# Performance work log

Hardware: AMD Instinct MI355X
Metric: run time of the kernel (lower is better)

## Reference

```python
import jax, jax.numpy as jnp
import numpy as np

B, L, D, H, R, E = 4, 2048, 256, 4, 128, 32768
HD = D // H  # head dim of long-range attention
FF = 4 * D   # positionwise FFN hidden
NEG_SLOPE = 0.2  # GATConv leaky_relu slope


def setup_inputs() -> dict:
    key = jax.random.key(0)
    ks = jax.random.split(key, 16)
    n = lambda k, sh: jax.random.normal(k, sh, dtype=jnp.float32) * 0.05
    z = lambda sh: jnp.zeros(sh, dtype=jnp.float32)
    o = lambda sh: jnp.ones(sh, dtype=jnp.float32)
    return {
        "s": jax.random.normal(ks[0], (B, L, D), dtype=jnp.float32),
        "gat_W": n(ks[1], (D, H * D)),
        "gat_att_src": n(ks[2], (H, D)),
        "gat_att_dst": n(ks[3], (H, D)),
        "gat_b": z((H * D,)),
        "short_W": n(ks[4], (H * D, D)), "short_b": z((D,)),
        "q_W": n(ks[5], (D, D)), "q_b": z((D,)),
        "k_W": n(ks[6], (D, D)), "k_b": z((D,)),
        "v_W": n(ks[7], (D, D)), "v_b": z((D,)),
        "o_W": n(ks[8], (D, D)), "o_b": z((D,)),
        "p_W": n(ks[9], (D, R)), "p_b": z((R,)),
        "lnq_g": o((D,)), "lnq_b": z((D,)),
        "lnk_g": o((D,)), "lnk_b": z((D,)),
        "lnv_g": o((D,)), "lnv_b": z((D,)),
        "ln1_g": o((D,)), "ln1_b": z((D,)),
        "ln2_g": o((D,)), "ln2_b": z((D,)),
        "f1_W": n(ks[10], (D, FF)), "f1_b": z((FF,)),
        "f2_W": n(ks[11], (FF, D)), "f2_b": z((D,)),
        "edge_index": jax.random.randint(ks[12], (2, E), 0, L, dtype=jnp.int32),
    }


def _ln(x, g, b, eps=1e-5):
    mu = jnp.mean(x, -1, keepdims=True)
    var = jnp.mean(jnp.square(x - mu), -1, keepdims=True)
    return (x - mu) * jax.lax.rsqrt(var + eps) * g + b


def _forward(p, edge_index):
    s = p["s"]
    loop = jnp.arange(L, dtype=edge_index.dtype)  # add_self_loops=True
    src = jnp.concatenate([edge_index[0], loop])
    dst = jnp.concatenate([edge_index[1], loop])

    def gat_one(x):  # x: [L, D] -> [L, H*D]  (PyG GATConv, concat=True)
        h = (x @ p["gat_W"]).reshape(L, H, D)
        a_src = jnp.einsum("nhc,hc->nh", h, p["gat_att_src"])
        a_dst = jnp.einsum("nhc,hc->nh", h, p["gat_att_dst"])
        e = jax.nn.leaky_relu(a_src[src] + a_dst[dst], NEG_SLOPE)  # [Etot, H]
        m = jax.ops.segment_max(e, dst, num_segments=L)            # scatter softmax
        ex = jnp.exp(e - m[dst])
        den = jax.ops.segment_sum(ex, dst, num_segments=L)
        alpha = ex / den[dst]
        out = jax.ops.segment_sum(h[src] * alpha[:, :, None], dst, num_segments=L)
        return out.reshape(L, H * D) + p["gat_b"]

    short = jax.vmap(gat_one)(s) @ p["short_W"] + p["short_b"]  # [B,L,D]

    # DynamicLongRange (Linformer-style dynamic projection)
    q = _ln(s @ p["q_W"] + p["q_b"], p["lnq_g"], p["lnq_b"])
    k = _ln(s @ p["k_W"] + p["k_b"], p["lnk_g"], p["lnk_b"])
    v = _ln(s @ p["v_W"] + p["v_b"], p["lnv_g"], p["lnv_b"])
    pm = jax.nn.softmax(k @ p["p_W"] + p["p_b"], axis=1)          # [B,L,R], softmax over seq
    k_c = jnp.einsum("blr,bld->brd", pm, k).reshape(B, R, H, HD)
    v_c = jnp.einsum("blr,bld->brd", pm, v).reshape(B, R, H, HD)
    q_h = q.reshape(B, L, H, HD)
    scores = jnp.einsum("blhd,brhd->bhlr", q_h, k_c) / jnp.sqrt(jnp.float32(HD))
    probs = jax.nn.softmax(scores, axis=-1)
    lng = jnp.einsum("bhlr,brhd->blhd", probs, v_c).reshape(B, L, D)
    lng = lng @ p["o_W"] + p["o_b"]

    # fuse short + long, residual + LN, then positionwise FFN + residual + LN
    h1 = _ln(s + short + lng, p["ln1_g"], p["ln1_b"])
    ff = jax.nn.relu(h1 @ p["f1_W"] + p["f1_b"]) @ p["f2_W"] + p["f2_b"]
    return _ln(h1 + ff, p["ln2_g"], p["ln2_b"])


def reference(s, gat_W, gat_att_src, gat_att_dst, gat_b, short_W, short_b,
              q_W, q_b, k_W, k_b, v_W, v_b, o_W, o_b, p_W, p_b,
              lnq_g, lnq_b, lnk_g, lnk_b, lnv_g, lnv_b,
              ln1_g, ln1_b, ln2_g, ln2_b, f1_W, f1_b, f2_W, f2_b, edge_index):
    p = dict(s=s, gat_W=gat_W, gat_att_src=gat_att_src, gat_att_dst=gat_att_dst,
             gat_b=gat_b, short_W=short_W, short_b=short_b, q_W=q_W, q_b=q_b,
             k_W=k_W, k_b=k_b, v_W=v_W, v_b=v_b, o_W=o_W, o_b=o_b, p_W=p_W,
             p_b=p_b, lnq_g=lnq_g, lnq_b=lnq_b, lnk_g=lnk_g, lnk_b=lnk_b,
             lnv_g=lnv_g, lnv_b=lnv_b, ln1_g=ln1_g, ln1_b=ln1_b, ln2_g=ln2_g,
             ln2_b=ln2_b, f1_W=f1_W, f1_b=f1_b, f2_W=f2_W, f2_b=f2_b)
    return _forward(p, edge_index)
```

## Files before the change

### kernel.cpp

```cpp
#include <hip/hip_runtime.h>
#include <math.h>

#define BB   4
#define LSEQ 2048
#define DV   256
#define HH   4
#define RR   128
#define EE   32768
#define ETOT (EE + LSEQ)
#define FFD  1024

typedef unsigned short u16;
typedef __attribute__((ext_vector_type(8))) short bf16x8;
typedef __attribute__((ext_vector_type(4))) float f32x4;

__device__ __forceinline__ u16 f2bf(float f) {
    union { float f; unsigned u; } x; x.f = f;
    unsigned r = x.u + 0x7fff + ((x.u >> 16) & 1);
    return (u16)(r >> 16);
}
__device__ __forceinline__ float bf2f(u16 u) {
    union { unsigned u; float f; } x; x.u = ((unsigned)u) << 16;
    return x.f;
}

__device__ __forceinline__ void gload16(const void* g, void* l) {
    __builtin_amdgcn_global_load_lds(
        (const __attribute__((address_space(1))) unsigned int*)g,
        (__attribute__((address_space(3))) unsigned int*)l, 16, 0, 0);
}

template<int BM, int BN, int OUTBF16, int ACT>
__global__ __launch_bounds__(256) void mfma_gemm_k(
    const u16* __restrict__ A, const u16* __restrict__ BT,
    const float* __restrict__ bias, void* __restrict__ Cv,
    int M, int N, int K, int lda, int ldb, int ldc,
    long bsA1, long bsA2, long bsB1, long bsB2, long bsC1, long bsC2,
    int subH, long pairB, long pairC, int ksl, int split, float alpha)
{
    constexpr int BK = 64;
    __shared__ u16 As[BM * BK];
    __shared__ u16 Bs[BN * BK];

    int z = blockIdx.z;
    int zb = z / subH, zh = z - zb * subH;
    int mtiles = M / BM;
    int pair = blockIdx.y / mtiles;
    int mt   = blockIdx.y - pair * mtiles;

    const u16* Ab = A  + zb * bsA1 + zh * bsA2;
    const u16* Bb = BT + zb * bsB1 + zh * bsB2 + (long)pair * pairB;
    int kstart = split ? zh * ksl : 0;
    int kcount = split ? ksl : K;
    int m0 = mt * BM, n0 = blockIdx.x * BN;

    int tid  = threadIdx.x;
    int wave = tid >> 6, lane = tid & 63;
    constexpr int WGN = (BN == 128) ? 2 : 1;
    constexpr int WGM = 4 / WGN;
    constexpr int MI  = BM / (WGM * 16);
    constexpr int NI  = BN / (WGN * 16);
    int wm = wave / WGN, wn = wave - wm * WGN;
    int wmo = wm * (MI * 16);
    int wno = wn * (NI * 16);

    f32x4 acc[MI][NI];
#pragma unroll
    for (int mi = 0; mi < MI; ++mi)
#pragma unroll
        for (int ni = 0; ni < NI; ++ni)
            acc[mi][ni] = (f32x4){0.f, 0.f, 0.f, 0.f};

    constexpr int AIT = (BM * BK / 8) / 256;
    constexpr int BIT = (BN * BK / 8) / 256;

    for (int k0 = 0; k0 < kcount; k0 += BK) {
        int kb = kstart + k0;
#pragma unroll
        for (int i = 0; i < AIT; ++i) {
            int p   = i * 256 + tid;
            int row = p >> 3;
            int kc  = (p & 7) ^ (row & 7);
            const u16* gp = Ab + (long)(m0 + row) * lda + kb + kc * 8;
            gload16(gp, (char*)As + (size_t)(i * 256 + wave * 64) * 16);
        }
#pragma unroll
        for (int i = 0; i < BIT; ++i) {
            int p   = i * 256 + tid;
            int row = p >> 3;
            int kc  = (p & 7) ^ (row & 7);
            const u16* gp = Bb + (long)(n0 + row) * ldb + kb + kc * 8;
            gload16(gp, (char*)Bs + (size_t)(i * 256 + wave * 64) * 16);
        }
        asm volatile("s_waitcnt vmcnt(0)");
        __syncthreads();

        const char* Ac = (const char*)As;
        const char* Bc = (const char*)Bs;
#pragma unroll
        for (int kh = 0; kh < 2; ++kh) {
            bf16x8 af[MI], bfr[NI];
            int kby = kh * 64 + ((lane >> 4) << 4);
#pragma unroll
            for (int mi = 0; mi < MI; ++mi) {
                int r = wmo + mi * 16 + (lane & 15);
                af[mi] = *(const bf16x8*)(Ac + r * 128 + (kby ^ ((r & 7) << 4)));
            }
#pragma unroll
            for (int ni = 0; ni < NI; ++ni) {
                int r = wno + ni * 16 + (lane & 15);
                bfr[ni] = *(const bf16x8*)(Bc + r * 128 + (kby ^ ((r & 7) << 4)));
            }
#pragma unroll
            for (int mi = 0; mi < MI; ++mi)
#pragma unroll
                for (int ni = 0; ni < NI; ++ni)
                    acc[mi][ni] = __builtin_amdgcn_mfma_f32_16x16x32_bf16(
                        af[mi], bfr[ni], acc[mi][ni], 0, 0, 0);
        }
        __syncthreads();
    }

    long cb = zb * bsC1 + zh * bsC2 + (long)pair * pairC;
#pragma unroll
    for (int mi = 0; mi < MI; ++mi) {
#pragma unroll
        for (int ni = 0; ni < NI; ++ni) {
            int col = n0 + wno + ni * 16 + (lane & 15);
            float bv = bias ? bias[col] : 0.f;
#pragma unroll
            for (int j = 0; j < 4; ++j) {
                int row = m0 + wmo + mi * 16 + ((lane >> 4) << 2) + j;
                float v = acc[mi][ni][j] * alpha + bv;
                if (ACT) v = fmaxf(v, 0.f);
                long idx = (long)row * ldc + col + cb;
                if (OUTBF16) ((u16*)Cv)[idx] = f2bf(v);
                else         ((float*)Cv)[idx] = v;
            }
        }
    }
}

template<int MODE>
__global__ __launch_bounds__(256) void gemm_ln_k(
    const u16* __restrict__ A, const u16* __restrict__ BT,
    const float* __restrict__ bias, int K, int lda,
    const float* __restrict__ lg0, const float* __restrict__ lb0,
    const float* __restrict__ lg1, const float* __restrict__ lb1,
    const float* __restrict__ lg2, const float* __restrict__ lb2,
    const float* __restrict__ resF, const u16* __restrict__ resB,
    u16* __restrict__ outRM, u16* __restrict__ outRM2,
    u16* __restrict__ outT, float* __restrict__ outF)
{
    constexpr int BK = 64;
    __shared__ char smem[40960];
    __shared__ float redS[64][4], redQ[64][4];
    u16* Asm = (u16*)smem;
    u16* Bsm = (u16*)(smem + 8192);

    int seg = blockIdx.x;
    int m0 = blockIdx.y * 64;
    int n0 = seg * 256;
    int tid = threadIdx.x, wave = tid >> 6, lane = tid & 63;
    int c = lane & 15, g = lane >> 4;

    f32x4 acc[4][4];
#pragma unroll
    for (int mi = 0; mi < 4; ++mi)
#pragma unroll
        for (int ni = 0; ni < 4; ++ni)
            acc[mi][ni] = (f32x4){0.f, 0.f, 0.f, 0.f};

    for (int k0 = 0; k0 < K; k0 += BK) {
#pragma unroll
        for (int i = 0; i < 2; ++i) {
            int p   = i * 256 + tid;
            int row = p >> 3;
            int kc  = (p & 7) ^ (row & 7);
            gload16(A + (long)(m0 + row) * lda + k0 + kc * 8,
                    smem + (size_t)(i * 256 + wave * 64) * 16);
        }
#pragma unroll
        for (int i = 0; i < 8; ++i) {
            int p   = i * 256 + tid;
            int row = p >> 3;
            int kc  = (p & 7) ^ (row & 7);
            gload16(BT + (long)(n0 + row) * K + k0 + kc * 8,
                    smem + 8192 + (size_t)(i * 256 + wave * 64) * 16);
        }
        asm volatile("s_waitcnt vmcnt(0)");
        __syncthreads();

        const char* Ac = (const char*)Asm;
        const char* Bc = (const char*)Bsm;
#pragma unroll
        for (int kh = 0; kh < 2; ++kh) {
            bf16x8 af[4], bfr[4];
            int kby = kh * 64 + (g << 4);
#pragma unroll
            for (int mi = 0; mi < 4; ++mi) {
                int r = mi * 16 + c;
                af[mi] = *(const bf16x8*)(Ac + r * 128 + (kby ^ ((r & 7) << 4)));
            }
#pragma unroll
            for (int ni = 0; ni < 4; ++ni) {
                int r = wave * 64 + ni * 16 + c;
                bfr[ni] = *(const bf16x8*)(Bc + r * 128 + (kby ^ ((r & 7) << 4)));
            }
#pragma unroll
            for (int mi = 0; mi < 4; ++mi)
#pragma unroll
                for (int ni = 0; ni < 4; ++ni)
                    acc[mi][ni] = __builtin_amdgcn_mfma_f32_16x16x32_bf16(
                        af[mi], bfr[ni], acc[mi][ni], 0, 0, 0);
        }
        __syncthreads();
    }

#pragma unroll
    for (int mi = 0; mi < 4; ++mi)
#pragma unroll
        for (int ni = 0; ni < 4; ++ni) {
            int colL = wave * 64 + ni * 16 + c;
            float bv = bias[n0 + colL];
#pragma unroll
            for (int j = 0; j < 4; ++j) {
                int row = mi * 16 + g * 4 + j;
                float v = acc[mi][ni][j] + bv;
                if (MODE == 1) {
                    long idx = (long)(m0 + row) * 256 + colL;
                    v += resF[idx] + bf2f(resB[idx]);
                }
                if (MODE == 2) {
                    long idx = (long)(m0 + row) * 256 + colL;
                    v += bf2f(resB[idx]);
                }
                acc[mi][ni][j] = v;
            }
        }

#pragma unroll
    for (int mi = 0; mi < 4; ++mi)
#pragma unroll
        for (int j = 0; j < 4; ++j) {
            float s1 = 0.f, q1 = 0.f;
#pragma unroll
            for (int ni = 0; ni < 4; ++ni) {
                float v = acc[mi][ni][j];
                s1 += v; q1 += v * v;
            }
#pragma unroll
            for (int m = 1; m <= 8; m <<= 1) {
                s1 += __shfl_xor(s1, m);
                q1 += __shfl_xor(q1, m);
            }
            if (c == 0) {
                int row = mi * 16 + g * 4 + j;
                redS[row][wave] = s1;
                redQ[row][wave] = q1;
            }
        }
    __syncthreads();

    const float* gam;
    const float* bet;
    if (MODE == 0) {
        gam = (seg == 0) ? lg0 : (seg == 1) ? lg1 : lg2;
        bet = (seg == 0) ? lb0 : (seg == 1) ? lb1 : lb2;
    } else { gam = lg0; bet = lb0; }

    u16* T = (u16*)smem;

    float gv[4], bv2[4];
#pragma unroll
    for (int ni = 0; ni < 4; ++ni) {
        int colL = wave * 64 + ni * 16 + c;
        gv[ni] = gam[colL];
        bv2[ni] = bet[colL];
    }

#pragma unroll
    for (int mi = 0; mi < 4; ++mi)
#pragma unroll
        for (int j = 0; j < 4; ++j) {
            int row = mi * 16 + g * 4 + j;
            float S = redS[row][0] + redS[row][1] + redS[row][2] + redS[row][3];
            float Q = redQ[row][0] + redQ[row][1] + redQ[row][2] + redQ[row][3];
            float mu = S * (1.0f / 256.f);
            float var = Q * (1.0f / 256.f) - mu * mu;
            float rs = rsqrtf(var + 1e-5f);
#pragma unroll
            for (int ni = 0; ni < 4; ++ni) {
                int colL = wave * 64 + ni * 16 + c;
                float o = (acc[mi][ni][j] - mu) * rs * gv[ni] + bv2[ni];
                long idx = (long)(m0 + row) * 256 + colL;
                if (MODE == 0) {
                    u16 ob = f2bf(o);
                    if (seg == 0)      outRM[idx]  = ob;
                    else if (seg == 1) { outRM2[idx] = ob; T[colL * 65 + row] = ob; }
                    else               T[colL * 65 + row] = ob;
                } else if (MODE == 1) {
                    outRM[idx] = f2bf(o);
                } else {
                    outF[idx] = o;
                }
            }
        }

    if (MODE == 0 && seg >= 1) {
        __syncthreads();
        int b = m0 >> 11;
        int l0 = m0 & 2047;
        u16* dst = outT + ((seg == 2) ? 2097152 : 0)
                 + (long)b * 524288 + (long)tid * 2048 + l0;
        const u16* src = T + tid * 65;
#pragma unroll
        for (int i = 0; i < 8; ++i) {
            u16 tmp[8];
#pragma unroll
            for (int k2 = 0; k2 < 8; ++k2) tmp[k2] = src[i * 8 + k2];
            *(uint4*)(dst + i * 8) = *(uint4*)tmp;
        }
    }
}

__global__ __launch_bounds__(256) void attn_k(
    const u16* __restrict__ qb, const u16* __restrict__ kcb,
    const u16* __restrict__ vcT, u16* __restrict__ lngb)
{
    __shared__ u16 Ps[64 * 128];

    int bh = blockIdx.y;
    int b = bh >> 2, h = bh & 3;
    int l0 = blockIdx.x * 64;
    int tid = threadIdx.x, wave = tid >> 6, lane = tid & 63;
    int c = lane & 15, g = lane >> 4;

    const u16* kc = kcb + (long)b * (RR * DV) + h * 64;
    const u16* qg = qb + ((long)(b * LSEQ + l0)) * DV + h * 64;
    const u16* vg = vcT + ((long)b * DV + h * 64) * RR;

    f32x4 acc[8];
#pragma unroll
    for (int mi = 0; mi < 8; ++mi) acc[mi] = (f32x4){0.f, 0.f, 0.f, 0.f};

#pragma unroll
    for (int kh = 0; kh < 2; ++kh) {
        bf16x8 bq = *(const bf16x8*)(qg + (long)(wave * 16 + c) * DV + kh * 32 + g * 8);
#pragma unroll
        for (int mi = 0; mi < 8; ++mi) {
            bf16x8 af = *(const bf16x8*)(kc + (long)(mi * 16 + c) * DV + kh * 32 + g * 8);
            acc[mi] = __builtin_amdgcn_mfma_f32_16x16x32_bf16(af, bq, acc[mi], 0, 0, 0);
        }
    }

    float mx = -INFINITY;
#pragma unroll
    for (int mi = 0; mi < 8; ++mi)
#pragma unroll
        for (int j = 0; j < 4; ++j) {
            acc[mi][j] *= 0.125f;
            mx = fmaxf(mx, acc[mi][j]);
        }
    mx = fmaxf(mx, __shfl_xor(mx, 16));
    mx = fmaxf(mx, __shfl_xor(mx, 32));
    float den = 0.f;
#pragma unroll
    for (int mi = 0; mi < 8; ++mi)
#pragma unroll
        for (int j = 0; j < 4; ++j) {
            acc[mi][j] = __expf(acc[mi][j] - mx);
            den += acc[mi][j];
        }
    den += __shfl_xor(den, 16);
    den += __shfl_xor(den, 32);
    float inv = 1.0f / den;

    int l = wave * 16 + c;
#pragma unroll
    for (int mi = 0; mi < 8; ++mi) {
        short4 sv;
        sv.x = (short)f2bf(acc[mi][0] * inv);
        sv.y = (short)f2bf(acc[mi][1] * inv);
        sv.z = (short)f2bf(acc[mi][2] * inv);
        sv.w = (short)f2bf(acc[mi][3] * inv);
        int byte = l * 256 + ((mi * 32 + g * 8) ^ ((l & 7) << 4));
        *(short4*)((char*)Ps + byte) = sv;
    }
    __syncthreads();

    f32x4 a2[4];
#pragma unroll
    for (int ni = 0; ni < 4; ++ni) a2[ni] = (f32x4){0.f, 0.f, 0.f, 0.f};
#pragma unroll
    for (int kb = 0; kb < 4; ++kb) {
        int kby = kb * 64 + (g << 4);
        bf16x8 pa = *(const bf16x8*)((char*)Ps + l * 256 + (kby ^ ((l & 7) << 4)));
#pragma unroll
        for (int ni = 0; ni < 4; ++ni) {
            bf16x8 vf = *(const bf16x8*)(vg + (long)(ni * 16 + c) * RR + kb * 32 + g * 8);
            a2[ni] = __builtin_amdgcn_mfma_f32_16x16x32_bf16(pa, vf, a2[ni], 0, 0, 0);
        }
    }
#pragma unroll
    for (int ni = 0; ni < 4; ++ni)
#pragma unroll
        for (int j = 0; j < 4; ++j) {
            int lr = wave * 16 + g * 4 + j;
            int dh = ni * 16 + c;
            lngb[((long)(b * LSEQ + l0 + lr)) * DV + h * 64 + dh] = f2bf(a2[ni][j]);
        }
}

struct WTD { const float* src; u16* dst; int K, N, toff; };
struct WTA { WTD d[9]; };

__global__ __launch_bounds__(256) void wtrans_all_k(WTA a)
{
    int bid = blockIdx.x;
    int di = 0;
#pragma unroll
    for (int i = 1; i < 9; ++i) if (bid >= a.d[i].toff) di = i;
    const float* src = a.d[di].src;
    u16* dst = a.d[di].dst;
    int K = a.d[di].K, N = a.d[di].N;
    int tix = bid - a.d[di].toff;
    int nx = N >> 5;
    int tn = tix % nx, tk = tix / nx;
    int n0 = tn * 32, k0 = tk * 32;

    __shared__ float t[32][33];
    int tx = threadIdx.x & 31, ty = threadIdx.x >> 5;
#pragma unroll
    for (int i = 0; i < 32; i += 8)
        t[ty + i][tx] = src[(long)(k0 + ty + i) * N + n0 + tx];
    __syncthreads();
#pragma unroll
    for (int i = 0; i < 32; i += 8)
        dst[(long)(n0 + ty + i) * K + k0 + tx] = f2bf(t[tx][ty + i]);
}

__global__ void castcat_k(const float* __restrict__ in, u16* __restrict__ out,
                          const float* qb_, const float* kb_, const float* vb_,
                          float* qkvb, int* icnt)
{
    int bid = blockIdx.x;
    if (bid < 2048) {
        int i = (bid * 256 + threadIdx.x) * 4;
        float4 v = *(const float4*)(in + i);
        out[i]     = f2bf(v.x);
        out[i + 1] = f2bf(v.y);
        out[i + 2] = f2bf(v.z);
        out[i + 3] = f2bf(v.w);
    } else if (bid == 2048) {
        int i = threadIdx.x;
#pragma unroll
        for (int rep = 0; rep < 3; ++rep) {
            int j = i + rep * 256;
            qkvb[j] = (j < 256) ? qb_[j] : ((j < 512) ? kb_[j - 256] : vb_[j - 512]);
        }
    } else {
        int t = (bid - 2049) * 256 + threadIdx.x;
        if (t < 512) ((int4*)icnt)[t] = (int4){0, 0, 0, 0};
    }
}

__global__ __launch_bounds__(256) void gat_att_k(
    const u16* __restrict__ h, const float* __restrict__ att_src,
    const float* __restrict__ att_dst, float* __restrict__ a_src,
    float* __restrict__ a_dst)
{
    int row  = blockIdx.x * 4 + (threadIdx.x >> 6);
    int lane = threadIdx.x & 63;
    int c0   = lane * 16;
    int head = lane >> 4;

    float as[16], ad[16];
#pragma unroll
    for (int i = 0; i < 16; ++i) { as[i] = att_src[c0 + i]; ad[i] = att_dst[c0 + i]; }

    const u16* hr = h + (long)row * (HH * DV) + c0;
    bf16x8 v0 = *(const bf16x8*)(hr);
    bf16x8 v1 = *(const bf16x8*)(hr + 8);
    float ps = 0.f, pd = 0.f;
#pragma unroll
    for (int i = 0; i < 8; ++i) {
        float f0 = bf2f((u16)v0[i]), f1 = bf2f((u16)v1[i]);
        ps += f0 * as[i] + f1 * as[i + 8];
        pd += f0 * ad[i] + f1 * ad[i + 8];
    }
#pragma unroll
    for (int m = 1; m <= 8; m <<= 1) {
        ps += __shfl_xor(ps, m);
        pd += __shfl_xor(pd, m);
    }
    if ((lane & 15) == 0) {
        a_src[(long)row * HH + head] = ps;
        a_dst[(long)row * HH + head] = pd;
    }
}

__global__ void csr_count_k(const int* __restrict__ ei, int* __restrict__ cnt)
{
    int i = blockIdx.x * blockDim.x + threadIdx.x;
    if (i >= ETOT) return;
    int dst = (i < EE) ? ei[EE + i] : (i - EE);
    atomicAdd(&cnt[dst], 1);
}

__global__ __launch_bounds__(256) void csr_scan_k(const int* __restrict__ cnt, int* __restrict__ off)
{
    __shared__ int chunk[256];
    int tid = threadIdx.x;
    int base = tid * 8;
    int loc[8];
    int s = 0;
#pragma unroll
    for (int i = 0; i < 8; ++i) { loc[i] = s; s += cnt[base + i]; }
    chunk[tid] = s;
    __syncthreads();
    for (int st = 1; st < 256; st <<= 1) {
        int v = (tid >= st) ? chunk[tid - st] : 0;
        __syncthreads();
        chunk[tid] += v;
        __syncthreads();
    }
    int pre = (tid == 0) ? 0 : chunk[tid - 1];
#pragma unroll
    for (int i = 0; i < 8; ++i) off[base + i] = pre + loc[i];
    if (tid == 255) off[LSEQ] = chunk[255];
}

__global__ void csr_fill_k(const int* __restrict__ ei, const int* __restrict__ off,
                           int* __restrict__ cnt, int* __restrict__ bucket)
{
    int i = blockIdx.x * blockDim.x + threadIdx.x;
    if (i >= ETOT) return;
    int dst = (i < EE) ? ei[EE + i] : (i - EE);
    int p = atomicSub(&cnt[dst], 1) - 1;
    bucket[off[dst] + p] = i;
}

__global__ __launch_bounds__(256) void gat_gather_k(
    const u16* __restrict__ h, const int* __restrict__ ei,
    const int* __restrict__ off, const int* __restrict__ bucket,
    const float* __restrict__ a_src, const float* __restrict__ a_dst,
    const float* __restrict__ gat_b, u16* __restrict__ out)
{
    int wv = threadIdx.x >> 6, lane = threadIdx.x & 63;
    int n = blockIdx.x * 4 + wv;
    int b = blockIdx.y;
    int beg = off[n], deg = off[n + 1] - beg;

    __shared__ int   src_sh[4][64];
    __shared__ float ex_sh[4][64][4];

    const float* asrc_b = a_src + (long)b * LSEQ * HH;
    const float4 ad4 = *(const float4*)(a_dst + ((long)b * LSEQ + n) * HH);
    float adst[4] = { ad4.x, ad4.y, ad4.z, ad4.w };

    int hd = lane >> 4;
    const u16* hb = h + (long)b * LSEQ * (HH * DV) + lane * 16;
    float acc[16];
#pragma unroll
    for (int i = 0; i < 16; ++i) acc[i] = 0.f;
    float sm[4] = { 0.f, 0.f, 0.f, 0.f };

    for (int c0 = 0; c0 < deg; c0 += 64) {
        int idx = c0 + lane;
        if (idx < deg) {
            int eid = bucket[beg + idx];
            int src = (eid < EE) ? ei[eid] : (eid - EE);
            src_sh[wv][lane] = src;
            float4 as4 = *(const float4*)(asrc_b + (long)src * HH);
            float as[4] = { as4.x, as4.y, as4.z, as4.w };
#pragma unroll
            for (int hh = 0; hh < 4; ++hh) {
                float e = as[hh] + adst[hh];
                e = (e >= 0.f) ? e : 0.2f * e;
                float ex = __expf(e);
                ex_sh[wv][lane][hh] = ex;
                sm[hh] += ex;
            }
        }
        int cn = deg - c0; if (cn > 64) cn = 64;
#pragma unroll 2
        for (int j = 0; j < cn; ++j) {
            int src = src_sh[wv][j];
            float al = ex_sh[wv][j][hd];
            const u16* p = hb + (long)src * (HH * DV);
            bf16x8 v0 = *(const bf16x8*)p;
            bf16x8 v1 = *(const bf16x8*)(p + 8);
#pragma unroll
            for (int i = 0; i < 8; ++i) {
                acc[i]     += al * bf2f((u16)v0[i]);
                acc[i + 8] += al * bf2f((u16)v1[i]);
            }
        }
    }

#pragma unroll
    for (int hh = 0; hh < 4; ++hh)
#pragma unroll
        for (int m = 32; m >= 1; m >>= 1)
            sm[hh] += __shfl_xor(sm[hh], m);
    float inv = 1.0f / sm[hd];

    u16 o16[16];
    const float* gb = gat_b + lane * 16;
#pragma unroll
    for (int i = 0; i < 16; ++i) o16[i] = f2bf(acc[i] * inv + gb[i]);
    uint4* op = (uint4*)(out + ((long)b * LSEQ + n) * (HH * DV) + lane * 16);
    op[0] = ((uint4*)o16)[0];
    op[1] = ((uint4*)o16)[1];
}

__global__ __launch_bounds__(256) void colsoftmax_k(const float* __restrict__ pm,
                                                    u16* __restrict__ pmT)
{
    int r = blockIdx.x;
    int b = blockIdx.y;
    int tid = threadIdx.x, wave = tid >> 6, lane = tid & 63;
    const float* base = pm + (long)b * LSEQ * RR + r;
    u16* obase = pmT + ((long)b * RR + r) * LSEQ;

    float x[8];
#pragma unroll
    for (int i = 0; i < 8; ++i) x[i] = base[(long)(tid + i * 256) * RR];

    __shared__ float red[4];
    __shared__ float m_sh, d_sh;
    float mx = x[0];
#pragma unroll
    for (int i = 1; i < 8; ++i) mx = fmaxf(mx, x[i]);
#pragma unroll
    for (int m = 32; m >= 1; m >>= 1) mx = fmaxf(mx, __shfl_xor(mx, m));
    if (lane == 0) red[wave] = mx;
    __syncthreads();
    if (tid == 0) m_sh = fmaxf(fmaxf(red[0], red[1]), fmaxf(red[2], red[3]));
    __syncthreads();
    float m = m_sh;
    float sm = 0.f;
#pragma unroll
    for (int i = 0; i < 8; ++i) { x[i] = __expf(x[i] - m); sm += x[i]; }
#pragma unroll
    for (int mm = 32; mm >= 1; mm >>= 1) sm += __shfl_xor(sm, mm);
    if (lane == 0) red[wave] = sm;
    __syncthreads();
    if (tid == 0) d_sh = red[0] + red[1] + red[2] + red[3];
    __syncthreads();
    float inv = 1.0f / d_sh;
#pragma unroll
    for (int i = 0; i < 8; ++i) obase[tid + i * 256] = f2bf(x[i] * inv);
}

__global__ __launch_bounds__(256) void reduce_kvc_k(
    const float* __restrict__ part, u16* __restrict__ kvcb, u16* __restrict__ vcT)
{
    int pb = blockIdx.z;
    int pair = pb >> 2, b = pb & 3;
    int r0 = blockIdx.y * 32, d0 = blockIdx.x * 64;
    int tid = threadIdx.x;
    __shared__ float t[32][65];
    const float* pp = part + (long)pb * (16 * 32768);
    int r = tid >> 6;
    int d = tid & 63;
#pragma unroll
    for (int i = 0; i < 8; ++i) {
        int rr = r0 + r + i * 4;
        float s = 0.f;
#pragma unroll
        for (int sp = 0; sp < 16; ++sp)
            s += pp[(long)sp * 32768 + rr * 256 + d0 + d];
        kvcb[(long)pb * 32768 + rr * 256 + d0 + d] = f2bf(s);
        t[r + i * 4][d] = s;
    }
    if (pair == 0) return;
    __syncthreads();
    int dd = tid >> 2, rb = (tid & 3) * 8;
    u16 o8[8];
#pragma unroll
    for (int k = 0; k < 8; ++k) o8[k] = f2bf(t[rb + k][dd]);
    *(uint4*)(vcT + ((long)(b * 256 + d0 + dd)) * 128 + r0 + rb) = *(uint4*)o8;
}

extern "C" void kernel_launch(void* const* d_in, const int* in_sizes, int n_in,
                              void* d_out, int out_size, void* d_ws, size_t ws_size,
                              hipStream_t stream)
{
    const float* s        = (const float*)d_in[0];
    const float* gat_W    = (const float*)d_in[1];
    const float* att_src  = (const float*)d_in[2];
    const float* att_dst  = (const float*)d_in[3];
    const float* gat_b    = (const float*)d_in[4];
    const float* short_W  = (const float*)d_in[5];
    const float* short_b  = (const float*)d_in[6];
    const float* q_W      = (const float*)d_in[7];
    const float* q_b      = (const float*)d_in[8];
    const float* k_W      = (const float*)d_in[9];
    const float* k_b      = (const float*)d_in[10];
    const float* v_W      = (const float*)d_in[11];
    const float* v_b      = (const float*)d_in[12];
    const float* o_W      = (const float*)d_in[13];
    const float* o_b      = (const float*)d_in[14];
    const float* p_W      = (const float*)d_in[15];
    const float* p_b      = (const float*)d_in[16];
    const float* lnq_g    = (const float*)d_in[17];
    const float* lnq_b    = (const float*)d_in[18];
    const float* lnk_g    = (const float*)d_in[19];
    const float* lnk_b    = (const float*)d_in[20];
    const float* lnv_g    = (const float*)d_in[21];
    const float* lnv_b    = (const float*)d_in[22];
    const float* ln1_g    = (const float*)d_in[23];
    const float* ln1_b    = (const float*)d_in[24];
    const float* ln2_g    = (const float*)d_in[25];
    const float* ln2_b    = (const float*)d_in[26];
    const float* f1_W     = (const float*)d_in[27];
    const float* f1_b     = (const float*)d_in[28];
    const float* f2_W     = (const float*)d_in[29];
    const float* f2_b     = (const float*)d_in[30];
    const int*   ei       = (const int*)d_in[31];
    float* out = (float*)d_out;

    const size_t MB = 1024 * 1024;
    char* W = (char*)d_ws;
    u16*   sb      = (u16*)(W);
    u16*   gatT    = (u16*)(W + 4*MB);
    u16*   shortT  = (u16*)(W + 4*MB + 524288);
    u16*   qkvT    = (u16*)(W + 4*MB + 1048576);
    u16*   oT      = (u16*)(W + 4*MB + 1441792);
    u16*   pT      = (u16*)(W + 4*MB + 1572864);
    u16*   f1T     = (u16*)(W + 4*MB + 1638400);
    u16*   f2T     = (u16*)(W + 4*MB + 2162688);
    float* qkvb    = (float*)(W + 4*MB + 2686976);
    int*   ioff    = (int*)(W + 4*MB + 2690048);
    int*   icnt    = (int*)(W + 4*MB + 2699264);
    int*   ibucket = (int*)(W + 4*MB + 2707456);
    u16*   h       = (u16*)(W + 8*MB);
    u16*   ffh     = (u16*)(W + 8*MB);
    u16*   gat_out = (u16*)(W + 24*MB);
    u16*   h1b     = (u16*)(W + 40*MB);
    u16*   shortb16= (u16*)(W + 44*MB);
    float* pmraw   = (float*)(W + 48*MB);
    float* part    = (float*)(W + 48*MB);
    u16*   lngb    = (u16*)(W + 48*MB);
    u16*   qb      = (u16*)(W + 72*MB);
    u16*   kb      = (u16*)(W + 76*MB);
    u16*   kvT     = (u16*)(W + 84*MB);
    u16*   pmT     = (u16*)(W + 92*MB);
    u16*   kvcb    = (u16*)(W + 94*MB);
    u16*   vcT     = (u16*)(W + 94*MB + 524288);
    float* a_src   = (float*)(W + 95*MB);
    float* a_dst   = (float*)(W + 95*MB + 131072);

    const int ML = BB * LSEQ;

    WTA wa;
    wa.d[0] = { gat_W,   gatT,            256, 1024, 0    };
    wa.d[1] = { short_W, shortT,         1024,  256, 256  };
    wa.d[2] = { q_W,     qkvT,            256,  256, 512  };
    wa.d[3] = { k_W,     qkvT + 65536,    256,  256, 576  };
    wa.d[4] = { v_W,     qkvT + 131072,   256,  256, 640  };
    wa.d[5] = { o_W,     oT,              256,  256, 704  };
    wa.d[6] = { p_W,     pT,              256,  128, 768  };
    wa.d[7] = { f1_W,    f1T,             256, 1024, 800  };
    wa.d[8] = { f2_W,    f2T,            1024,  256, 1056 };
    wtrans_all_k<<<1312, 256, 0, stream>>>(wa);
    castcat_k<<<2051, 256, 0, stream>>>(s, sb, q_b, k_b, v_b, qkvb, icnt);

    csr_count_k<<<(ETOT + 255) / 256, 256, 0, stream>>>(ei, icnt);
    csr_scan_k<<<1, 256, 0, stream>>>(icnt, ioff);
    csr_fill_k<<<(ETOT + 255) / 256, 256, 0, stream>>>(ei, ioff, icnt, ibucket);

    mfma_gemm_k<128, 128, 1, 0><<<dim3(8, 64, 1), 256, 0, stream>>>(
        sb, gatT, nullptr, h, ML, 1024, 256, 256, 256, 1024,
        0, 0, 0, 0, 0, 0, 1, 0, 0, 0, 0, 1.f);
    gat_att_k<<<ML / 4, 256, 0, stream>>>(h, att_src, att_dst, a_src, a_dst);
    gat_gather_k<<<dim3(LSEQ / 4, BB), 256, 0, stream>>>(h, ei, ioff, ibucket,
                                                         a_src, a_dst, gat_b, gat_out);
    mfma_gemm_k<64, 128, 1, 0><<<dim3(2, 128, 1), 256, 0, stream>>>(
        gat_out, shortT, short_b, shortb16, ML, 256, 1024, 1024, 1024, 256,
        0, 0, 0, 0, 0, 0, 1, 0, 0, 0, 0, 1.f);

    gemm_ln_k<0><<<dim3(3, 128), 256, 0, stream>>>(
        sb, qkvT, qkvb, 256, 256,
        lnq_g, lnq_b, lnk_g, lnk_b, lnv_g, lnv_b,
        nullptr, nullptr, qb, kb, kvT, nullptr);

    mfma_gemm_k<64, 64, 0, 0><<<dim3(2, 128, 1), 256, 0, stream>>>(
        kb, pT, p_b, pmraw, ML, 128, 256, 256, 256, 128,
        0, 0, 0, 0, 0, 0, 1, 0, 0, 0, 0, 1.f);
    colsoftmax_k<<<dim3(RR, BB), 256, 0, stream>>>(pmraw, pmT);

    mfma_gemm_k<128, 128, 0, 0><<<dim3(2, 2, 64), 256, 0, stream>>>(
        pmT, kvT, nullptr, part, 128, 256, 2048, 2048, 2048, 256,
        262144, 0, 524288, 0, 524288, 32768, 16, 2097152, 2097152, 128, 1, 1.f);
    reduce_kvc_k<<<dim3(4, 4, 8), 256, 0, stream>>>(part, kvcb, vcT);

    attn_k<<<dim3(LSEQ / 64, BB * HH), 256, 0, stream>>>(qb, kvcb, vcT, lngb);

    gemm_ln_k<1><<<dim3(1, 128), 256, 0, stream>>>(
        lngb, oT, o_b, 256, 256,
        ln1_g, ln1_b, nullptr, nullptr, nullptr, nullptr,
        s, shortb16, h1b, nullptr, nullptr, nullptr);

    mfma_gemm_k<128, 128, 1, 1><<<dim3(8, 64, 1), 256, 0, stream>>>(
        h1b, f1T, f1_b, ffh, ML, 1024, 256, 256, 256, 1024,
        0, 0, 0, 0, 0, 0, 1, 0, 0, 0, 0, 1.f);

    gemm_ln_k<2><<<dim3(1, 128), 256, 0, stream>>>(
        ffh, f2T, f2_b, 1024, 1024,
        ln2_g, ln2_b, nullptr, nullptr, nullptr, nullptr,
        nullptr, h1b, nullptr, nullptr, nullptr, out);
}
```

Before: 220.0 us.

## Merge prep kernels, shrink LN-GEMM row tiles, reorder GAT gather grid, use bf16 residual

```diff
diff --git a/kernel.cpp b/kernel.cpp
--- a/kernel.cpp
+++ b/kernel.cpp
@@ -141,39 +141,43 @@
     }
 }
 
-template<int MODE>
+template<int MODE, int BM>
 __global__ __launch_bounds__(256) void gemm_ln_k(
     const u16* __restrict__ A, const u16* __restrict__ BT,
     const float* __restrict__ bias, int K, int lda,
     const float* __restrict__ lg0, const float* __restrict__ lb0,
     const float* __restrict__ lg1, const float* __restrict__ lb1,
     const float* __restrict__ lg2, const float* __restrict__ lb2,
-    const float* __restrict__ resF, const u16* __restrict__ resB,
+    const u16* __restrict__ resB0, const u16* __restrict__ resB1,
     u16* __restrict__ outRM, u16* __restrict__ outRM2,
     u16* __restrict__ outT, float* __restrict__ outF)
 {
     constexpr int BK = 64;
-    __shared__ char smem[40960];
-    __shared__ float redS[64][4], redQ[64][4];
+    constexpr int MI = BM / 16;
+    constexpr int ABYTES = BM * 128;
+    __shared__ char smem[ABYTES + 32768];
+    __shared__ float redS[BM][4], redQ[BM][4];
     u16* Asm = (u16*)smem;
-    u16* Bsm = (u16*)(smem + 8192);
+    u16* Bsm = (u16*)(smem + ABYTES);
 
     int seg = blockIdx.x;
-    int m0 = blockIdx.y * 64;
+    int m0 = blockIdx.y * BM;
     int n0 = seg * 256;
     int tid = threadIdx.x, wave = tid >> 6, lane = tid & 63;
     int c = lane & 15, g = lane >> 4;
 
-    f32x4 acc[4][4];
-#pragma unroll
-    for (int mi = 0; mi < 4; ++mi)
+    f32x4 acc[MI][4];
+#pragma unroll
+    for (int mi = 0; mi < MI; ++mi)
 #pragma unroll
         for (int ni = 0; ni < 4; ++ni)
             acc[mi][ni] = (f32x4){0.f, 0.f, 0.f, 0.f};
 
+    constexpr int AIT = (BM * BK / 8) / 256;
+
     for (int k0 = 0; k0 < K; k0 += BK) {
 #pragma unroll
-        for (int i = 0; i < 2; ++i) {
+        for (int i = 0; i < AIT; ++i) {
             int p   = i * 256 + tid;
             int row = p >> 3;
             int kc  = (p & 7) ^ (row & 7);
@@ -186,7 +190,7 @@
             int row = p >> 3;
             int kc  = (p & 7) ^ (row & 7);
             gload16(BT + (long)(n0 + row) * K + k0 + kc * 8,
-                    smem + 8192 + (size_t)(i * 256 + wave * 64) * 16);
+                    smem + ABYTES + (size_t)(i * 256 + wave * 64) * 16);
         }
         asm volatile("s_waitcnt vmcnt(0)");
         __syncthreads();
@@ -195,10 +199,10 @@
         const char* Bc = (const char*)Bsm;
 #pragma unroll
         for (int kh = 0; kh < 2; ++kh) {
-            bf16x8 af[4], bfr[4];
+            bf16x8 af[MI], bfr[4];
             int kby = kh * 64 + (g << 4);
 #pragma unroll
-            for (int mi = 0; mi < 4; ++mi) {
+            for (int mi = 0; mi < MI; ++mi) {
                 int r = mi * 16 + c;
                 af[mi] = *(const bf16x8*)(Ac + r * 128 + (kby ^ ((r & 7) << 4)));
             }
@@ -208,7 +212,7 @@
                 bfr[ni] = *(const bf16x8*)(Bc + r * 128 + (kby ^ ((r & 7) << 4)));
             }
 #pragma unroll
-            for (int mi = 0; mi < 4; ++mi)
+            for (int mi = 0; mi < MI; ++mi)
 #pragma unroll
                 for (int ni = 0; ni < 4; ++ni)
                     acc[mi][ni] = __builtin_amdgcn_mfma_f32_16x16x32_bf16(
@@ -218,7 +222,7 @@
     }
 
 #pragma unroll
-    for (int mi = 0; mi < 4; ++mi)
+    for (int mi = 0; mi < MI; ++mi)
 #pragma unroll
         for (int ni = 0; ni < 4; ++ni) {
             int colL = wave * 64 + ni * 16 + c;
@@ -229,18 +233,18 @@
                 float v = acc[mi][ni][j] + bv;
                 if (MODE == 1) {
                     long idx = (long)(m0 + row) * 256 + colL;
-                    v += resF[idx] + bf2f(resB[idx]);
+                    v += bf2f(resB0[idx]) + bf2f(resB1[idx]);
                 }
                 if (MODE == 2) {
                     long idx = (long)(m0 + row) * 256 + colL;
-                    v += bf2f(resB[idx]);
+                    v += bf2f(resB0[idx]);
                 }
                 acc[mi][ni][j] = v;
             }
         }
 
 #pragma unroll
-    for (int mi = 0; mi < 4; ++mi)
+    for (int mi = 0; mi < MI; ++mi)
 #pragma unroll
         for (int j = 0; j < 4; ++j) {
             float s1 = 0.f, q1 = 0.f;
@@ -280,7 +284,7 @@
     }
 
 #pragma unroll
-    for (int mi = 0; mi < 4; ++mi)
+    for (int mi = 0; mi < MI; ++mi)
 #pragma unroll
         for (int j = 0; j < 4; ++j) {
             int row = mi * 16 + g * 4 + j;
@@ -415,44 +419,41 @@
 struct WTD { const float* src; u16* dst; int K, N, toff; };
 struct WTA { WTD d[9]; };
 
-__global__ __launch_bounds__(256) void wtrans_all_k(WTA a)
+__global__ __launch_bounds__(256) void prep_k(WTA a,
+    const float* __restrict__ sin, u16* __restrict__ sout,
+    const float* qb_, const float* kb_, const float* vb_,
+    float* qkvb, int* icnt)
 {
     int bid = blockIdx.x;
-    int di = 0;
-#pragma unroll
-    for (int i = 1; i < 9; ++i) if (bid >= a.d[i].toff) di = i;
-    const float* src = a.d[di].src;
-    u16* dst = a.d[di].dst;
-    int K = a.d[di].K, N = a.d[di].N;
-    int tix = bid - a.d[di].toff;
-    int nx = N >> 5;
-    int tn = tix % nx, tk = tix / nx;
-    int n0 = tn * 32, k0 = tk * 32;
-
-    __shared__ float t[32][33];
-    int tx = threadIdx.x & 31, ty = threadIdx.x >> 5;
-#pragma unroll
-    for (int i = 0; i < 32; i += 8)
-        t[ty + i][tx] = src[(long)(k0 + ty + i) * N + n0 + tx];
-    __syncthreads();
-#pragma unroll
-    for (int i = 0; i < 32; i += 8)
-        dst[(long)(n0 + ty + i) * K + k0 + tx] = f2bf(t[tx][ty + i]);
-}
-
-__global__ void castcat_k(const float* __restrict__ in, u16* __restrict__ out,
-                          const float* qb_, const float* kb_, const float* vb_,
-                          float* qkvb, int* icnt)
-{
-    int bid = blockIdx.x;
-    if (bid < 2048) {
-        int i = (bid * 256 + threadIdx.x) * 4;
-        float4 v = *(const float4*)(in + i);
-        out[i]     = f2bf(v.x);
-        out[i + 1] = f2bf(v.y);
-        out[i + 2] = f2bf(v.z);
-        out[i + 3] = f2bf(v.w);
-    } else if (bid == 2048) {
+    if (bid < 1312) {
+        int di = 0;
+#pragma unroll
+        for (int i = 1; i < 9; ++i) if (bid >= a.d[i].toff) di = i;
+        const float* src = a.d[di].src;
+        u16* dst = a.d[di].dst;
+        int K = a.d[di].K, N = a.d[di].N;
+        int tix = bid - a.d[di].toff;
+        int nx = N >> 5;
+        int tn = tix % nx, tk = tix / nx;
+        int n0 = tn * 32, k0 = tk * 32;
+
+        __shared__ float t[32][33];
+        int tx = threadIdx.x & 31, ty = threadIdx.x >> 5;
+#pragma unroll
+        for (int i = 0; i < 32; i += 8)
+            t[ty + i][tx] = src[(long)(k0 + ty + i) * N + n0 + tx];
+        __syncthreads();
+#pragma unroll
+        for (int i = 0; i < 32; i += 8)
+            dst[(long)(n0 + ty + i) * K + k0 + tx] = f2bf(t[tx][ty + i]);
+    } else if (bid < 3360) {
+        int i = ((bid - 1312) * 256 + threadIdx.x) * 4;
+        float4 v = *(const float4*)(sin + i);
+        sout[i]     = f2bf(v.x);
+        sout[i + 1] = f2bf(v.y);
+        sout[i + 2] = f2bf(v.z);
+        sout[i + 3] = f2bf(v.w);
+    } else if (bid == 3360) {
         int i = threadIdx.x;
 #pragma unroll
         for (int rep = 0; rep < 3; ++rep) {
@@ -460,7 +461,7 @@
             qkvb[j] = (j < 256) ? qb_[j] : ((j < 512) ? kb_[j - 256] : vb_[j - 512]);
         }
     } else {
-        int t = (bid - 2049) * 256 + threadIdx.x;
+        int t = (bid - 3361) * 256 + threadIdx.x;
         if (t < 512) ((int4*)icnt)[t] = (int4){0, 0, 0, 0};
     }
 }
@@ -548,8 +549,10 @@
     const float* __restrict__ gat_b, u16* __restrict__ out)
 {
     int wv = threadIdx.x >> 6, lane = threadIdx.x & 63;
-    int n = blockIdx.x * 4 + wv;
-    int b = blockIdx.y;
+    int id = blockIdx.x;
+    int jg = id >> 3, r8 = id & 7;
+    int b  = r8 >> 1;
+    int n  = (jg * 2 + (r8 & 1)) * 4 + wv;
     int beg = off[n], deg = off[n + 1] - beg;
 
     __shared__ int   src_sh[4][64];
@@ -765,8 +768,7 @@
     wa.d[6] = { p_W,     pT,              256,  128, 768  };
     wa.d[7] = { f1_W,    f1T,             256, 1024, 800  };
     wa.d[8] = { f2_W,    f2T,            1024,  256, 1056 };
-    wtrans_all_k<<<1312, 256, 0, stream>>>(wa);
-    castcat_k<<<2051, 256, 0, stream>>>(s, sb, q_b, k_b, v_b, qkvb, icnt);
+    prep_k<<<3363, 256, 0, stream>>>(wa, s, sb, q_b, k_b, v_b, qkvb, icnt);
 
     csr_count_k<<<(ETOT + 255) / 256, 256, 0, stream>>>(ei, icnt);
     csr_scan_k<<<1, 256, 0, stream>>>(icnt, ioff);
@@ -776,13 +778,13 @@
         sb, gatT, nullptr, h, ML, 1024, 256, 256, 256, 1024,
         0, 0, 0, 0, 0, 0, 1, 0, 0, 0, 0, 1.f);
     gat_att_k<<<ML / 4, 256, 0, stream>>>(h, att_src, att_dst, a_src, a_dst);
-    gat_gather_k<<<dim3(LSEQ / 4, BB), 256, 0, stream>>>(h, ei, ioff, ibucket,
-                                                         a_src, a_dst, gat_b, gat_out);
+    gat_gather_k<<<2048, 256, 0, stream>>>(h, ei, ioff, ibucket,
+                                           a_src, a_dst, gat_b, gat_out);
     mfma_gemm_k<64, 128, 1, 0><<<dim3(2, 128, 1), 256, 0, stream>>>(
         gat_out, shortT, short_b, shortb16, ML, 256, 1024, 1024, 1024, 256,
         0, 0, 0, 0, 0, 0, 1, 0, 0, 0, 0, 1.f);
 
-    gemm_ln_k<0><<<dim3(3, 128), 256, 0, stream>>>(
+    gemm_ln_k<0, 64><<<dim3(3, 128), 256, 0, stream>>>(
         sb, qkvT, qkvb, 256, 256,
         lnq_g, lnq_b, lnk_g, lnk_b, lnv_g, lnv_b,
         nullptr, nullptr, qb, kb, kvT, nullptr);
@@ -799,17 +801,17 @@
 
     attn_k<<<dim3(LSEQ / 64, BB * HH), 256, 0, stream>>>(qb, kvcb, vcT, lngb);
 
-    gemm_ln_k<1><<<dim3(1, 128), 256, 0, stream>>>(
+    gemm_ln_k<1, 32><<<dim3(1, 256), 256, 0, stream>>>(
         lngb, oT, o_b, 256, 256,
         ln1_g, ln1_b, nullptr, nullptr, nullptr, nullptr,
-        s, shortb16, h1b, nullptr, nullptr, nullptr);
+        sb, shortb16, h1b, nullptr, nullptr, nullptr);
 
     mfma_gemm_k<128, 128, 1, 1><<<dim3(8, 64, 1), 256, 0, stream>>>(
         h1b, f1T, f1_b, ffh, ML, 1024, 256, 256, 256, 1024,
         0, 0, 0, 0, 0, 0, 1, 0, 0, 0, 0, 1.f);
 
-    gemm_ln_k<2><<<dim3(1, 128), 256, 0, stream>>>(
+    gemm_ln_k<2, 32><<<dim3(1, 256), 256, 0, stream>>>(
         ffh, f2T, f2_b, 1024, 1024,
         ln2_g, ln2_b, nullptr, nullptr, nullptr, nullptr,
-        nullptr, h1b, nullptr, nullptr, nullptr, out);
-}
+        h1b, nullptr, nullptr, nullptr, nullptr, out);
+}
```

Result: faster. 195.4 us (median of 2 runs) (-11.2%).
